# Performance work log

Hardware: AMD Instinct MI355X
Metric: run time of the kernel (lower is better)

The kernel has to match this reference:

```python
import jax, jax.numpy as jnp
import numpy as np

VQ_ALPHA = 0.5   # non-trainable vq_alpha weight, constant 0.5
BETA = 0.25      # commitment loss weight


def setup_inputs() -> dict:
    key = jax.random.key(0)
    k1, k2 = jax.random.split(key)
    x = jax.random.normal(k1, (16, 64, 64, 256), dtype=jnp.float32)
    # tf.keras RandomUniform default is U(-0.05, 0.05)
    dictionary = jax.random.uniform(k2, (256, 1024), dtype=jnp.float32,
                                    minval=-0.05, maxval=0.05)
    return {"x": x, "dictionary": dictionary}


def reference(x, dictionary):
    D, K = dictionary.shape  # embedding_dim, num_embeddings
    flat = x.reshape(-1, D)  # [N, D]

    # squared L2 distances: ||f||^2 + ||d||^2 - 2 f.d   -> [N, K]
    similarity = flat @ dictionary
    distances = (jnp.sum(flat * flat, axis=1, keepdims=True)
                 + jnp.sum(dictionary * dictionary, axis=0, keepdims=True)
                 - 2.0 * similarity)
    code_idx = jnp.argmin(distances, axis=1)  # [N]

    # one-hot @ dict^T is just a row gather of dict^T
    quantized = jnp.take(dictionary.T, code_idx, axis=0)  # [N, D]
    quantized = VQ_ALPHA * quantized
    q = quantized.reshape(x.shape)

    dictionary_loss = jnp.mean(jnp.square(jax.lax.stop_gradient(x) - q))
    commitment_loss = jnp.mean(jnp.square(x - jax.lax.stop_gradient(q)))
    loss = dictionary_loss + BETA * commitment_loss

    # straight-through estimator
    q_st = x + jax.lax.stop_gradient(q - x)
    return q_st, loss
```

## Files before the change

### kernel.cpp

```cpp
#include <hip/hip_runtime.h>


#define NROWS   65536
#define DIM     256
#define NCODE   1024
#define RPB     64
#define NBLK    (NROWS / RPB)
#define NCHUNK  32
#define EPS_TIE 6e-3f

typedef _Float16 half8 __attribute__((ext_vector_type(8)));
typedef float    f32x4 __attribute__((ext_vector_type(4)));

__global__ void k_prep(const float* __restrict__ dict, float* __restrict__ dictT,
                       float* __restrict__ dictnorm, unsigned short* __restrict__ packB) {
    int gid = blockIdx.x * 256 + threadIdx.x;
#pragma unroll
    for (int ii = 0; ii < 4; ++ii) {
        int e = ii * 65536 + gid;
        const float v = dict[e];
        const int d = e >> 10, k = e & 1023;
        dictT[k * DIM + d] = v;
        _Float16 h = (_Float16)v;
        const int o = (k >> 5) * 8192 + ((d >> 5) * 2 + ((k >> 4) & 1)) * 512
                    + ((d >> 3) & 3) * 128 + (k & 15) * 8 + (d & 7);
        packB[o] = *(unsigned short*)&h;
    }
    if (blockIdx.x < 4) {
        int k = blockIdx.x * 256 + threadIdx.x;
        float s = 0.f;
#pragma unroll 8
        for (int d = 0; d < DIM; ++d) {
            float v = dict[d * NCODE + k];
            s = fmaf(v, v, s);
        }
        dictnorm[k] = s + 8.0f;
    }
}

__device__ __forceinline__ float np_pairwise_sq_128(const float* a, int stride) {
    float r[8];
#pragma unroll
    for (int j = 0; j < 8; ++j) {
        float v = a[j * stride];
        r[j] = __fmul_rn(v, v);
    }
    for (int i = 8; i < 128; i += 8) {
#pragma unroll
        for (int j = 0; j < 8; ++j) {
            float v = a[(i + j) * stride];
            r[j] = __fadd_rn(r[j], __fmul_rn(v, v));
        }
    }
    return __fadd_rn(__fadd_rn(__fadd_rn(r[0], r[1]), __fadd_rn(r[2], r[3])),
                     __fadd_rn(__fadd_rn(r[4], r[5]), __fadd_rn(r[6], r[7])));
}


#define STAGE(buf, cc) do {                                                            \
    const unsigned short* _s = packB + (size_t)(cc) * 8192 + tid * 8;                  \
    unsigned short* _d = &bstage[buf][tid * 8];                                        \
    _Pragma("unroll")                                                                  \
    for (int _p = 0; _p < 4; ++_p)                                                     \
        __builtin_amdgcn_global_load_lds(                                              \
            (const __attribute__((address_space(1))) unsigned int*)(_s + _p * 2048),   \
            (__attribute__((address_space(3))) unsigned int*)(_d + _p * 2048),         \
            16, 0, 0);                                                                 \
} while (0)

__global__ __launch_bounds__(256, 4) void k_vq(
    const float* __restrict__ x, const float* __restrict__ dict,
    const float* __restrict__ dictT, const float* __restrict__ dictnorm,
    const unsigned short* __restrict__ packB,
    float* __restrict__ out, double* __restrict__ block_sums)
{
    __shared__ __align__(16) unsigned short bstage[2][8192];
    __shared__ float row_gap[RPB];
    __shared__ int   row_k1[RPB];
    __shared__ float red_d[256];
    __shared__ int   red_k[256];
    __shared__ float wred[4];
    __shared__ int   amb_list[RPB];
    __shared__ int   amb_cnt;

    const int tid  = threadIdx.x;
    const int ln   = tid & 63, wv = tid >> 6;
    const int l15  = ln & 15, q = ln >> 4;
    const int row0 = blockIdx.x * RPB;

    STAGE(0, 0);
    if (tid == 0) amb_cnt = 0;

    half8 afrag[8];
    {
        const float* ar = x + (size_t)(row0 + wv * 16 + l15) * DIM + q * 8;
#pragma unroll
        for (int kk = 0; kk < 8; ++kk) {
            const float4 p0 = *(const float4*)(ar + kk * 32);
            const float4 p1 = *(const float4*)(ar + kk * 32 + 4);
            half8 h;
            h[0] = (_Float16)p0.x; h[1] = (_Float16)p0.y; h[2] = (_Float16)p0.z; h[3] = (_Float16)p0.w;
            h[4] = (_Float16)p1.x; h[5] = (_Float16)p1.y; h[6] = (_Float16)p1.z; h[7] = (_Float16)p1.w;
            afrag[kk] = h;
        }
    }

    unsigned p1v[4], p2v[4];
#pragma unroll
    for (int i = 0; i < 4; ++i) { p1v[i] = 0xFFFFFFFFu; p2v[i] = 0xFFFFFFFFu; }

    __syncthreads();

    for (int cc = 0; cc < NCHUNK; ++cc) {
        const int cur = cc & 1;
        if (cc < NCHUNK - 1) STAGE(cur ^ 1, cc + 1);
        const int c0 = cc * 32;
        float dn[2];
#pragma unroll
        for (int t = 0; t < 2; ++t) dn[t] = dictnorm[c0 + t * 16 + l15];

        const f32x4 zero = {0.f, 0.f, 0.f, 0.f};
        f32x4 acc[2];
        acc[0] = zero; acc[1] = zero;

#pragma unroll
        for (int kk = 0; kk < 8; ++kk) {
#pragma unroll
            for (int t = 0; t < 2; ++t) {
                const half8 b = *(const half8*)&bstage[cur][(kk * 2 + t) * 512 + q * 128 + l15 * 8];
                acc[t] = __builtin_amdgcn_mfma_f32_16x16x32_f16(afrag[kk], b, acc[t], 0, 0, 0);
            }
        }

#pragma unroll
        for (int t = 0; t < 2; ++t) {
            const unsigned kbase = (unsigned)(c0 + t * 16 + l15);
#pragma unroll
            for (int i = 0; i < 4; ++i) {
                const float s = fmaf(-2.f, acc[t][i], dn[t]);
                const unsigned pk = (__float_as_uint(s) & 0xFFFFFC00u) | kbase;
                const unsigned mx = p1v[i] > pk ? p1v[i] : pk;
                p2v[i] = p2v[i] < mx ? p2v[i] : mx;
                p1v[i] = p1v[i] < pk ? p1v[i] : pk;
            }
        }
        __syncthreads();
    }

#pragma unroll
    for (int i = 0; i < 4; ++i) {
        unsigned a1 = p1v[i], a2 = p2v[i];
#pragma unroll
        for (int m = 1; m < 16; m <<= 1) {
            const unsigned o1 = __shfl_xor(a1, m);
            const unsigned o2 = __shfl_xor(a2, m);
            const unsigned mx = a1 > o1 ? a1 : o1;
            a1 = a1 < o1 ? a1 : o1;
            const unsigned mn2 = a2 < o2 ? a2 : o2;
            a2 = mx < mn2 ? mx : mn2;
        }
        if (l15 == 0) {
            const int r = wv * 16 + q * 4 + i;
            row_k1[r]  = (int)(a1 & 1023u);
            row_gap[r] = __uint_as_float(a2 & 0xFFFFFC00u) - __uint_as_float(a1 & 0xFFFFFC00u);
        }
    }
    __syncthreads();

    if (tid < RPB && row_gap[tid] < EPS_TIE) {
        int p = atomicAdd(&amb_cnt, 1);
        amb_list[p] = tid;
    }
    __syncthreads();
    const int namb = amb_cnt;

    for (int a = 0; a < namb; ++a) {
        const int r = amb_list[a];
        const float* xr = x + (size_t)(row0 + r) * DIM;
        const float nf = __fadd_rn(np_pairwise_sq_128(xr, 1), np_pairwise_sq_128(xr + 128, 1));
        float bd = 3.4e38f; int bk = 0x7fffffff;
#pragma unroll
        for (int i = 0; i < 4; ++i) {
            const int k = i * 256 + tid;
            float sim = 0.f, nd = 0.f;
            for (int d = 0; d < DIM; ++d) {
                const float dv = dict[(size_t)d * NCODE + k];
                const float fv = xr[d];
                sim = fmaf(fv, dv, sim);
                nd  = __fadd_rn(nd, __fmul_rn(dv, dv));
            }
            const float dist = __fsub_rn(__fadd_rn(nf, nd), __fmul_rn(2.f, sim));
            if (dist < bd) { bd = dist; bk = k; }
        }
        red_d[tid] = bd; red_k[tid] = bk;
        __syncthreads();
        for (int s = 128; s > 0; s >>= 1) {
            if (tid < s) {
                const float od = red_d[tid + s]; const int ok = red_k[tid + s];
                if (od < red_d[tid] || (od == red_d[tid] && ok < red_k[tid])) {
                    red_d[tid] = od; red_k[tid] = ok;
                }
            }
            __syncthreads();
        }
        if (tid == 0) row_k1[r] = red_k[0];
        __syncthreads();
    }

    float lsum = 0.f;
#pragma unroll 2
    for (int i = 0; i < 16; ++i) {
        const int e = i * 1024 + tid * 4;
        const int r = e >> 8, d0 = e & 255;
        const int kk = row_k1[r];
        const float4 dv = *(const float4*)&dictT[(size_t)kk * DIM + d0];
        const float4 xv = *(const float4*)&x[(size_t)row0 * DIM + e];
        float4 qv; qv.x = 0.5f * dv.x; qv.y = 0.5f * dv.y; qv.z = 0.5f * dv.z; qv.w = 0.5f * dv.w;
        float4 ov;
        ov.x = __fadd_rn(xv.x, __fsub_rn(qv.x, xv.x));
        ov.y = __fadd_rn(xv.y, __fsub_rn(qv.y, xv.y));
        ov.z = __fadd_rn(xv.z, __fsub_rn(qv.z, xv.z));
        ov.w = __fadd_rn(xv.w, __fsub_rn(qv.w, xv.w));
        const float e0 = __fsub_rn(xv.x, qv.x), e1 = __fsub_rn(xv.y, qv.y);
        const float e2 = __fsub_rn(xv.z, qv.z), e3 = __fsub_rn(xv.w, qv.w);
        lsum += e0 * e0 + e1 * e1 + e2 * e2 + e3 * e3;
        *(float4*)&out[(size_t)row0 * DIM + e] = ov;
    }

#pragma unroll
    for (int sft = 32; sft > 0; sft >>= 1) lsum += __shfl_down(lsum, sft, 64);
    if ((tid & 63) == 0) wred[tid >> 6] = lsum;
    __syncthreads();
    if (tid == 0)
        block_sums[blockIdx.x] = (double)((wred[0] + wred[1]) + (wred[2] + wred[3]));
}


__global__ void k_finalize(const double* __restrict__ block_sums, float* __restrict__ out_loss) {
    __shared__ double w[16];
    const int t = threadIdx.x;
    double v = block_sums[t];
#pragma unroll
    for (int sft = 32; sft > 0; sft >>= 1) v += __shfl_down(v, sft, 64);
    if ((t & 63) == 0) w[t >> 6] = v;
    __syncthreads();
    if (t == 0) {
        double tot = 0.0;
        for (int i = 0; i < 16; ++i) tot += w[i];
        out_loss[0] = (float)(1.25 * tot / (double)(NROWS * DIM));
    }
}


extern "C" void kernel_launch(void* const* d_in, const int* in_sizes, int n_in,
                              void* d_out, int out_size, void* d_ws, size_t ws_size,
                              hipStream_t stream) {
    (void)in_sizes; (void)n_in; (void)out_size; (void)ws_size;
    const float* x    = (const float*)d_in[0];
    const float* dict = (const float*)d_in[1];
    float* out = (float*)d_out;

    char* ws = (char*)d_ws;
    float*          dictT      = (float*)ws;
    float*          dictnorm   = (float*)(ws + 1048576);
    double*         block_sums = (double*)(ws + 1048576 + 4096);
    unsigned short* packB      = (unsigned short*)(ws + 1048576 + 4096 + 8192);

    k_prep<<<256, 256, 0, stream>>>(dict, dictT, dictnorm, packB);
    k_vq<<<NBLK, 256, 0, stream>>>(x, dict, dictT, dictnorm, packB, out, block_sums);
    k_finalize<<<1, 1024, 0, stream>>>(block_sums, out + (size_t)NROWS * DIM);
}
```

Before: 335.0 us.

## Triple-buffer codebook staging with vmcnt waits and cache norms in LDS

New measurement: 324.5 us. 3.1% less time.

```diff
diff --git a/kernel.cpp b/kernel.cpp
--- a/kernel.cpp
+++ b/kernel.cpp
@@ -57,9 +57,9 @@
 }
 
 
-#define STAGE(buf, cc) do {                                                            \
+#define STAGE(bufptr, cc) do {                                                         \
     const unsigned short* _s = packB + (size_t)(cc) * 8192 + tid * 8;                  \
-    unsigned short* _d = &bstage[buf][tid * 8];                                        \
+    unsigned short* _d = (bufptr) + tid * 8;                                           \
     _Pragma("unroll")                                                                  \
     for (int _p = 0; _p < 4; ++_p)                                                     \
         __builtin_amdgcn_global_load_lds(                                              \
@@ -68,28 +68,61 @@
             16, 0, 0);                                                                 \
 } while (0)
 
-__global__ __launch_bounds__(256, 4) void k_vq(
+#define COMPUTE(cc, bs) do {                                                           \
+    const int _c0 = (cc) * 32;                                                         \
+    float _dn[2];                                                                      \
+    _dn[0] = dn_lds[_c0 + l15];                                                        \
+    _dn[1] = dn_lds[_c0 + 16 + l15];                                                   \
+    const f32x4 _zero = {0.f, 0.f, 0.f, 0.f};                                          \
+    f32x4 _acc[2]; _acc[0] = _zero; _acc[1] = _zero;                                   \
+    _Pragma("unroll")                                                                  \
+    for (int _kk = 0; _kk < 8; ++_kk) {                                                \
+        _Pragma("unroll")                                                              \
+        for (int _t = 0; _t < 2; ++_t) {                                               \
+            const half8 _b = *(const half8*)&(bs)[(_kk * 2 + _t) * 512 + q * 128 + l15 * 8]; \
+            _acc[_t] = __builtin_amdgcn_mfma_f32_16x16x32_f16(afrag[_kk], _b, _acc[_t], 0, 0, 0); \
+        }                                                                              \
+    }                                                                                  \
+    _Pragma("unroll")                                                                  \
+    for (int _t = 0; _t < 2; ++_t) {                                                   \
+        const unsigned _kbase = (unsigned)(_c0 + _t * 16 + l15);                       \
+        _Pragma("unroll")                                                              \
+        for (int _i = 0; _i < 4; ++_i) {                                               \
+            const float _s = fmaf(-2.f, _acc[_t][_i], _dn[_t]);                        \
+            const unsigned _pk = (__float_as_uint(_s) & 0xFFFFFC00u) | _kbase;         \
+            const unsigned _mx = p1v[_i] > _pk ? p1v[_i] : _pk;                        \
+            p2v[_i] = p2v[_i] < _mx ? p2v[_i] : _mx;                                   \
+            p1v[_i] = p1v[_i] < _pk ? p1v[_i] : _pk;                                   \
+        }                                                                              \
+    }                                                                                  \
+} while (0)
+
+__global__ __launch_bounds__(256, 3) void k_vq(
     const float* __restrict__ x, const float* __restrict__ dict,
     const float* __restrict__ dictT, const float* __restrict__ dictnorm,
     const unsigned short* __restrict__ packB,
     float* __restrict__ out, double* __restrict__ block_sums)
 {
-    __shared__ __align__(16) unsigned short bstage[2][8192];
-    __shared__ float row_gap[RPB];
-    __shared__ int   row_k1[RPB];
-    __shared__ float red_d[256];
-    __shared__ int   red_k[256];
-    __shared__ float wred[4];
-    __shared__ int   amb_list[RPB];
-    __shared__ int   amb_cnt;
+    __shared__ __align__(16) unsigned short bstage[3][8192];
+    __shared__ float dn_lds[NCODE];
+    float* red_d    = (float*)&bstage[0][0];
+    int*   red_k    = (int*)  &bstage[0][512];
+    float* row_gap  = (float*)&bstage[0][1024];
+    int*   row_k1   = (int*)  &bstage[0][1152];
+    float* wred     = (float*)&bstage[0][1280];
+    int*   amb_list = (int*)  &bstage[0][1288];
+    int*   amb_cnt  = (int*)  &bstage[0][1416];
 
     const int tid  = threadIdx.x;
     const int ln   = tid & 63, wv = tid >> 6;
     const int l15  = ln & 15, q = ln >> 4;
     const int row0 = blockIdx.x * RPB;
 
-    STAGE(0, 0);
-    if (tid == 0) amb_cnt = 0;
+    {
+        const float4 v = *(const float4*)&dictnorm[tid * 4];
+        *(float4*)&dn_lds[tid * 4] = v;
+    }
+    __syncthreads();
 
     half8 afrag[8];
     {
@@ -109,43 +142,29 @@
 #pragma unroll
     for (int i = 0; i < 4; ++i) { p1v[i] = 0xFFFFFFFFu; p2v[i] = 0xFFFFFFFFu; }
 
-    __syncthreads();
-
-    for (int cc = 0; cc < NCHUNK; ++cc) {
-        const int cur = cc & 1;
-        if (cc < NCHUNK - 1) STAGE(cur ^ 1, cc + 1);
-        const int c0 = cc * 32;
-        float dn[2];
-#pragma unroll
-        for (int t = 0; t < 2; ++t) dn[t] = dictnorm[c0 + t * 16 + l15];
-
-        const f32x4 zero = {0.f, 0.f, 0.f, 0.f};
-        f32x4 acc[2];
-        acc[0] = zero; acc[1] = zero;
-
-#pragma unroll
-        for (int kk = 0; kk < 8; ++kk) {
-#pragma unroll
-            for (int t = 0; t < 2; ++t) {
-                const half8 b = *(const half8*)&bstage[cur][(kk * 2 + t) * 512 + q * 128 + l15 * 8];
-                acc[t] = __builtin_amdgcn_mfma_f32_16x16x32_f16(afrag[kk], b, acc[t], 0, 0, 0);
-            }
-        }
-
-#pragma unroll
-        for (int t = 0; t < 2; ++t) {
-            const unsigned kbase = (unsigned)(c0 + t * 16 + l15);
-#pragma unroll
-            for (int i = 0; i < 4; ++i) {
-                const float s = fmaf(-2.f, acc[t][i], dn[t]);
-                const unsigned pk = (__float_as_uint(s) & 0xFFFFFC00u) | kbase;
-                const unsigned mx = p1v[i] > pk ? p1v[i] : pk;
-                p2v[i] = p2v[i] < mx ? p2v[i] : mx;
-                p1v[i] = p1v[i] < pk ? p1v[i] : pk;
-            }
-        }
-        __syncthreads();
-    }
+    unsigned short* bA = &bstage[0][0];
+    unsigned short* bB = &bstage[1][0];
+    unsigned short* bC = &bstage[2][0];
+    STAGE(bA, 0);
+    STAGE(bB, 1);
+    __builtin_amdgcn_sched_barrier(0);
+
+    for (int cc = 0; cc < NCHUNK - 1; ++cc) {
+        asm volatile("s_waitcnt vmcnt(4)" ::: "memory");
+        __builtin_amdgcn_s_barrier();
+        __builtin_amdgcn_sched_barrier(0);
+        if (cc + 2 < NCHUNK) STAGE(bC, cc + 2);
+        COMPUTE(cc, bA);
+        unsigned short* tmp = bA; bA = bB; bB = bC; bC = tmp;
+    }
+    {
+        asm volatile("s_waitcnt vmcnt(0)" ::: "memory");
+        __builtin_amdgcn_s_barrier();
+        __builtin_amdgcn_sched_barrier(0);
+        COMPUTE(NCHUNK - 1, bA);
+    }
+    __syncthreads();
+    if (tid == 0) *amb_cnt = 0;
 
 #pragma unroll
     for (int i = 0; i < 4; ++i) {
@@ -168,11 +187,11 @@
     __syncthreads();
 
     if (tid < RPB && row_gap[tid] < EPS_TIE) {
-        int p = atomicAdd(&amb_cnt, 1);
+        int p = atomicAdd(amb_cnt, 1);
         amb_list[p] = tid;
     }
     __syncthreads();
-    const int namb = amb_cnt;
+    const int namb = *amb_cnt;
 
     for (int a = 0; a < namb; ++a) {
         const int r = amb_list[a];
```
